# Kernel optimization log

Hardware: AMD Instinct MI355X
Metric: run time of the kernel (lower is better)

The kernel has to match this reference:

```python
import jax, jax.numpy as jnp
import numpy as np


def conv1x1(x, w, b):
    # 1x1 Conv2d: x [B,C,H,W], w [O,C], b [O] -> [B,O,H,W]
    return jnp.einsum('bchw,oc->bohw', x, w) + b[None, :, None, None]


def setup_inputs() -> dict:
    key = jax.random.key(0)
    ks = jax.random.split(key, 10)
    B, C, Ci, H, W = 4, 64, 32, 64, 64
    s = 0.05
    return {
        'supp_feature': jax.random.normal(ks[0], (B, C, H, W), jnp.float32),
        'ref_feature': jax.random.normal(ks[1], (B, C, H, W), jnp.float32),
        'theta_w': jax.random.normal(ks[2], (Ci, C), jnp.float32) * s,
        'theta_b': jax.random.normal(ks[3], (Ci,), jnp.float32) * s,
        'phi_w': jax.random.normal(ks[4], (Ci, C), jnp.float32) * s,
        'phi_b': jax.random.normal(ks[5], (Ci,), jnp.float32) * s,
        'g_w': jax.random.normal(ks[6], (Ci, C), jnp.float32) * s,
        'g_b': jax.random.normal(ks[7], (Ci,), jnp.float32) * s,
        'w_w': jax.random.normal(ks[8], (C, Ci), jnp.float32) * s,
        'w_b': jax.random.normal(ks[9], (C,), jnp.float32) * s,
    }


def reference(supp_feature, ref_feature, theta_w, theta_b, phi_w, phi_b,
              g_w, g_b, w_w, w_b):
    B, C, H, W = supp_feature.shape
    Ci = theta_w.shape[0]
    N = H * W
    theta_x = conv1x1(supp_feature, theta_w, theta_b).reshape(B, Ci, N)  # [B,Ci,N]
    phi_y = conv1x1(ref_feature, phi_w, phi_b).reshape(B, Ci, N)        # [B,Ci,M]
    g_y = conv1x1(ref_feature, g_w, g_b).reshape(B, Ci, N)              # [B,Ci,M]
    # f[b,n,m] = <theta_x[b,:,n], phi_y[b,:,m]>  (unscaled)
    f = jnp.einsum('bcn,bcm->bnm', theta_x, phi_y)
    # NOTE: softmax over dim=1 (the QUERY axis n), matching F.softmax(f, dim=1)
    f_div_C = jax.nn.softmax(f, axis=1)
    # x1[b,c,n] = sum_m f_div_C[b,n,m] * g_y[b,c,m]
    x1 = jnp.einsum('bnm,bcm->bcn', f_div_C, g_y).reshape(B, Ci, H, W)
    z = supp_feature + conv1x1(x1, w_w, w_b)
    return z
```

## Files before the change

kernel.cpp:

```cpp
#include <hip/hip_runtime.h>

#define C_ 64
#define CI_ 32
#define N_ 4096
#define LOG2E 1.4426950408889634f
#define NBLK 256

typedef __attribute__((ext_vector_type(8))) short bf16x8;
typedef __attribute__((ext_vector_type(4))) float f32x4;

__device__ __forceinline__ unsigned short f2bf_rne(float f) {
  unsigned u = __builtin_bit_cast(unsigned, f);
  unsigned r = (u + 0x7FFFu + ((u >> 16) & 1u)) >> 16;
  return (unsigned short)r;
}
__device__ __forceinline__ unsigned pack_bf2(float lo, float hi) {
  unsigned a = (__builtin_bit_cast(unsigned, lo) + 0x8000u) >> 16;
  unsigned b = (__builtin_bit_cast(unsigned, hi) + 0x8000u) & 0xFFFF0000u;
  return a | b;
}
__device__ __forceinline__ void dma16(const void* gp, const void* lp) {
  __builtin_amdgcn_global_load_lds(
      (const __attribute__((address_space(1))) unsigned*)(unsigned long long)gp,
      (__attribute__((address_space(3))) unsigned*)(unsigned)(unsigned long long)lp,
      16, 0, 0);
}

__device__ __forceinline__ void sync_grid(unsigned* base) {
  asm volatile("s_waitcnt vmcnt(0)" ::: "memory");
  __syncthreads();
  if (threadIdx.x == 0) {
    const int g = blockIdx.x & 7;
    __threadfence();
    __hip_atomic_fetch_add(&base[g * 32], 1u, __ATOMIC_RELAXED, __HIP_MEMORY_SCOPE_AGENT);
    unsigned sp = 0;
    if (blockIdx.x < 8) {
      while (__hip_atomic_load(&base[g * 32], __ATOMIC_RELAXED, __HIP_MEMORY_SCOPE_AGENT) < 32u) {
        __builtin_amdgcn_s_sleep(16);
        if (++sp > 60000u) break;
      }
      __hip_atomic_fetch_add(&base[512], 1u, __ATOMIC_RELAXED, __HIP_MEMORY_SCOPE_AGENT);
      sp = 0;
      while (__hip_atomic_load(&base[512], __ATOMIC_RELAXED, __HIP_MEMORY_SCOPE_AGENT) < 8u) {
        __builtin_amdgcn_s_sleep(16);
        if (++sp > 60000u) break;
      }
      __hip_atomic_store(&base[256 + g * 32], 1u, __ATOMIC_RELAXED, __HIP_MEMORY_SCOPE_AGENT);
    } else {
      while (__hip_atomic_load(&base[256 + g * 32], __ATOMIC_RELAXED, __HIP_MEMORY_SCOPE_AGENT) == 0u) {
        __builtin_amdgcn_s_sleep(16);
        if (++sp > 60000u) break;
      }
    }
  }
  __syncthreads();
}

__global__ __launch_bounds__(1024) void fused(
    const float* __restrict__ supp, const float* __restrict__ ref,
    const float* __restrict__ tw, const float* __restrict__ tb,
    const float* __restrict__ pw, const float* __restrict__ pb,
    const float* __restrict__ gw, const float* __restrict__ gb,
    const float* __restrict__ ww, const float* __restrict__ wb,
    unsigned short* __restrict__ theta, unsigned short* __restrict__ phi2,
    unsigned short* __restrict__ g2, float* __restrict__ den,
    unsigned short* __restrict__ ww2, unsigned* __restrict__ bar,
    float* __restrict__ out)
{
  __shared__ __align__(16) unsigned char LB[86016];
  const int tid = threadIdx.x;
  const int bid = blockIdx.x;
  const int lane = tid & 63;
  const int w = tid >> 6;
  const int row16 = lane & 15;
  const int quad = lane >> 4;

  {
    const int b = bid >> 6;
    const int n0 = (bid & 63) << 6;
    const int n = n0 + lane;
    float (*gL)[66] = (float (*)[66])LB;

    if (w < 12) {
      const int o = __builtin_amdgcn_readfirstlane(w & 3);
      const float *W, *bias, *src;
      if (w < 4)      { W = tw; bias = tb; src = supp; }
      else if (w < 8) { W = pw; bias = pb; src = ref; }
      else            { W = gw; bias = gb; src = ref; }
      const float* x = src + (size_t)b * (C_ * N_) + n;
      const float* Wo = W + o * 8 * C_;
      float acc[8];
#pragma unroll
      for (int k = 0; k < 8; k++) acc[k] = bias[o * 8 + k];
#pragma unroll 8
      for (int c = 0; c < C_; c++) {
        float v = x[(size_t)c * N_];
#pragma unroll
        for (int k = 0; k < 8; k++) acc[k] = fmaf(Wo[k * C_ + c], v, acc[k]);
      }
      if (w < 4) {
        unsigned pk[4];
#pragma unroll
        for (int k = 0; k < 4; k++)
          pk[k] = (unsigned)f2bf_rne(acc[2 * k] * LOG2E) |
                  ((unsigned)f2bf_rne(acc[2 * k + 1] * LOG2E) << 16);
        *(uint4*)(theta + (((size_t)b * N_ + n) << 5) + o * 8) = *(uint4*)pk;
      } else if (w < 8) {
        unsigned pk[4];
#pragma unroll
        for (int k = 0; k < 4; k++)
          pk[k] = (unsigned)f2bf_rne(acc[2 * k]) |
                  ((unsigned)f2bf_rne(acc[2 * k + 1]) << 16);
        size_t off = (((size_t)b * 128 + (n >> 5)) << 10) + o * 256 + (n & 31) * 8;
        *(uint4*)(phi2 + off) = *(uint4*)pk;
      } else {
#pragma unroll
        for (int k = 0; k < 8; k++) gL[o * 8 + k][lane] = acc[k];
      }
    } else if (bid == 16) {
      for (int e = tid - 768; e < C_ * CI_; e += 256) {
        int p = e & 31;
        int i = 4 * ((p >> 3) & 3) + (p & 3) + 16 * ((p >> 2) & 1);
        ww2[e] = f2bf_rne(ww[(e >> 5) * CI_ + i]);
      }
    }
    __syncthreads();
    if (tid < 256) {
      const int c = tid >> 7;
      const int rr2 = tid & 127;
      const int q = rr2 >> 5;
      const int i = rr2 & 31;
      const float* g0 = &gL[i][c * 32 + 4 * q];
      unsigned gk[4];
      gk[0] = pack_bf2(g0[0], g0[1]);
      gk[1] = pack_bf2(g0[2], g0[3]);
      gk[2] = pack_bf2(g0[16], g0[17]);
      gk[3] = pack_bf2(g0[18], g0[19]);
      size_t goff = (((size_t)b * 128 + (n0 >> 5) + c) << 10) + rr2 * 8;
      *(uint4*)(g2 + goff) = *(uint4*)gk;
    }
  }

  sync_grid(bar);

  {
    const int b = bid >> 6;
    const int mt = bid & 63;
    const int nq = w >> 2;
    const int ws = w & 3;
    unsigned short (*TH)[2][4096] = (unsigned short (*)[2][4096])LB;
    float* denL = (float*)(LB + 65536);

    bf16x8 bf = *(const bf16x8*)(phi2 +
        (((size_t)b * 128 + mt * 2 + (ws >> 1)) << 10) + (quad << 8) +
        ((ws & 1) * 16 + row16) * 8);

    const unsigned short* thbase = theta + (((size_t)b * N_ + nq * 1024) << 5);

#pragma unroll
    for (int s = 0; s < 2; s++)
      dma16(thbase + (ws * 2 + s) * 512 + lane * 8, &TH[nq][0][(ws * 2 + s) * 512]);
    __syncthreads();

    f32x4 zero = {0.f, 0.f, 0.f, 0.f};
    float ds4[4] = {0.f, 0.f, 0.f, 0.f};

    for (int ph = 0; ph < 8; ph++) {
      const int buf = ph & 1;
      if (ph + 1 < 8) {
#pragma unroll
        for (int s = 0; s < 2; s++)
          dma16(thbase + (ph + 1) * 4096 + (ws * 2 + s) * 512 + lane * 8,
                &TH[nq][buf ^ 1][(ws * 2 + s) * 512]);
      }
#pragma unroll
      for (int s = 0; s < 8; s++) {
        bf16x8 af = *(const bf16x8*)(&TH[nq][buf][s * 512 + row16 * 32 + quad * 8]);
        f32x4 ff = __builtin_amdgcn_mfma_f32_16x16x32_bf16(af, bf, zero, 0, 0, 0);
#pragma unroll
        for (int r = 0; r < 4; r++) ds4[r] += __builtin_amdgcn_exp2f(ff[r]);
      }
      __syncthreads();
    }

    float v = (ds4[0] + ds4[1]) + (ds4[2] + ds4[3]);
    v += __shfl_xor(v, 16);
    v += __shfl_xor(v, 32);
    if (lane < 16) denL[nq * 64 + ws * 16 + lane] = v;
    __syncthreads();
    if (tid < 64) {
      float sv = (denL[tid] + denL[64 + tid]) + (denL[128 + tid] + denL[192 + tid]);
      int ch = mt * 2 + (tid >> 5);
      int local = tid & 31;
      int qq = (local & 15) >> 2;
      int j = (local & 3) | (((local >> 4) & 1) << 2);
      den[(((size_t)b * 128 + ch) << 5) + 8 * qq + j] = sv;
    }
  }

  sync_grid(bar + 640);

  {
    const int p = bid;
    const int b = (p & 7) >> 1;
    const int t = ((p >> 3) << 1) | (p & 1);
    const int n0 = t << 6;
    const int ns = w & 3;
    const int q = w >> 2;
    unsigned short (*SB)[4][4096] = (unsigned short (*)[4][4096])LB;
    float* ldL = (float*)(LB + 65536);

    for (int e = tid; e < 4096; e += 1024)
      ldL[e] = -__log2f(den[((size_t)b << 12) + e]);

    bf16x8 tB = *(const bf16x8*)(theta +
        (((size_t)b * N_ + n0 + ns * 16 + row16) << 5) + (quad << 3));

    const size_t chb = (size_t)b * 128;
    const int sq = q;

    f32x4 zero = {0.f, 0.f, 0.f, 0.f};
    f32x4 xa = zero, xb = zero;

#pragma unroll
    for (int s = 0; s < 2; s++) {
      int idx = w * 2 + s;
      int cc = (idx >> 2) & 1;
      int part = idx & 3;
      const unsigned short* src = (part >= 2 ? g2 : phi2) +
          ((chb + sq * 32 + cc) << 10) + ((size_t)(part & 1) << 9) + lane * 8;
      dma16(src, &SB[0][sq][cc * 2048 + (part >= 2 ? 1024 : 0) + ((part & 1) << 9)]);
    }
    __syncthreads();

    for (int ph = 0; ph < 16; ph++) {
      const int buf = ph & 1;
      if (ph + 1 < 16) {
#pragma unroll
        for (int s = 0; s < 2; s++) {
          int idx = w * 2 + s;
          int cc = (idx >> 2) & 1;
          int part = idx & 3;
          const unsigned short* src = (part >= 2 ? g2 : phi2) +
              ((chb + sq * 32 + (ph + 1) * 2 + cc) << 10) + ((size_t)(part & 1) << 9) + lane * 8;
          dma16(src, &SB[buf ^ 1][sq][cc * 2048 + (part >= 2 ? 1024 : 0) + ((part & 1) << 9)]);
        }
      }
#pragma unroll
      for (int cc = 0; cc < 2; cc++) {
        const unsigned short* base = &SB[buf][q][cc * 2048];
        bf16x8 pA0 = *(const bf16x8*)(base + (quad << 8) + row16 * 8);
        bf16x8 pA1 = *(const bf16x8*)(base + (quad << 8) + (row16 + 16) * 8);
        bf16x8 gA0 = *(const bf16x8*)(base + 1024 + (quad << 8) + row16 * 8);
        bf16x8 gA1 = *(const bf16x8*)(base + 1024 + (quad << 8) + (row16 + 16) * 8);
        const float* lp = &ldL[((q * 32 + ph * 2 + cc) << 5) + (quad << 3)];
        f32x4 l0 = *(const f32x4*)lp;
        f32x4 l1 = *(const f32x4*)(lp + 4);

        f32x4 f0 = __builtin_amdgcn_mfma_f32_16x16x32_bf16(pA0, tB, l0, 0, 0, 0);
        f32x4 f1 = __builtin_amdgcn_mfma_f32_16x16x32_bf16(pA1, tB, l1, 0, 0, 0);

        uint4 d;
        d.x = pack_bf2(__builtin_amdgcn_exp2f(f0[0]), __builtin_amdgcn_exp2f(f0[1]));
        d.y = pack_bf2(__builtin_amdgcn_exp2f(f0[2]), __builtin_amdgcn_exp2f(f0[3]));
        d.z = pack_bf2(__builtin_amdgcn_exp2f(f1[0]), __builtin_amdgcn_exp2f(f1[1]));
        d.w = pack_bf2(__builtin_amdgcn_exp2f(f1[2]), __builtin_amdgcn_exp2f(f1[3]));
        bf16x8 Pb = __builtin_bit_cast(bf16x8, d);

        xa = __builtin_amdgcn_mfma_f32_16x16x32_bf16(gA0, Pb, xa, 0, 0, 0);
        xb = __builtin_amdgcn_mfma_f32_16x16x32_bf16(gA1, Pb, xb, 0, 0, 0);
      }
      __syncthreads();
    }

    float* part = (float*)LB;
    if (q) {
      float* dst = part + ((((q - 1) * 4 + ns) * 64 + lane) << 3);
#pragma unroll
      for (int r = 0; r < 4; r++) { dst[r] = xa[r]; dst[4 + r] = xb[r]; }
    }
    __syncthreads();
    if (q == 0) {
#pragma unroll
      for (int e = 0; e < 3; e++) {
        const float* s = part + (((e * 4 + ns) * 64 + lane) << 3);
#pragma unroll
        for (int r = 0; r < 4; r++) { xa[r] += s[r]; xb[r] += s[4 + r]; }
      }
      uint4 d;
      d.x = pack_bf2(xa[0], xa[1]);
      d.y = pack_bf2(xa[2], xa[3]);
      d.z = pack_bf2(xb[0], xb[1]);
      d.w = pack_bf2(xb[2], xb[3]);
      bf16x8 Bx = __builtin_bit_cast(bf16x8, d);
      const int nloc = n0 + ns * 16 + row16;
#pragma unroll
      for (int ct = 0; ct < 4; ct++) {
        bf16x8 aw = *(const bf16x8*)(ww2 + (ct * 16 + row16) * CI_ + (quad << 3));
        f32x4 o = __builtin_amdgcn_mfma_f32_16x16x32_bf16(aw, Bx, zero, 0, 0, 0);
#pragma unroll
        for (int r = 0; r < 4; r++) {
          int c = ct * 16 + quad * 4 + r;
          size_t ob = ((size_t)b * C_ + c) * N_ + nloc;
          out[ob] = o[r] + wb[c] + supp[ob];
        }
      }
    }
  }
}

extern "C" void kernel_launch(void* const* d_in, const int* in_sizes, int n_in,
                              void* d_out, int out_size, void* d_ws, size_t ws_size,
                              hipStream_t stream)
{
  const float* supp = (const float*)d_in[0];
  const float* ref  = (const float*)d_in[1];
  const float* tw   = (const float*)d_in[2];
  const float* tb   = (const float*)d_in[3];
  const float* pw   = (const float*)d_in[4];
  const float* pb   = (const float*)d_in[5];
  const float* gw   = (const float*)d_in[6];
  const float* gb   = (const float*)d_in[7];
  const float* ww   = (const float*)d_in[8];
  const float* wb   = (const float*)d_in[9];
  float* out = (float*)d_out;

  char* ws = (char*)d_ws;
  unsigned short* theta = (unsigned short*)ws;
  unsigned short* phi2  = (unsigned short*)(ws + (1u << 20));
  unsigned short* g2    = (unsigned short*)(ws + (2u << 20));
  float*          den   = (float*)(ws + (3u << 20));
  unsigned short* ww2   = (unsigned short*)(ws + (3u << 20) + 65536);
  unsigned*       bar   = (unsigned*)(ws + (3u << 20) + 65536 + 4096);

  hipMemsetAsync(bar, 0, 2 * 640 * sizeof(unsigned), stream);
  hipLaunchKernelGGL(fused, dim3(NBLK), dim3(1024), 0, stream,
                     supp, ref, tw, tb, pw, pb, gw, gb, ww, wb,
                     theta, phi2, g2, den, ww2, bar, out);
}
```

Baseline: 128.4 us.

## Add per-XCC fence stage to grid barrier and prefetch before second sync

Reworks the grid barrier. The per-block __threadfence is dropped, and one elected block per XCC waits for the release flag, issues a single fence and then joins a second counting round before blocks are released. Sleep intervals are shortened. The second barrier now comes after the first phi/g DMA and the theta load are issued, so those loads overlap the barrier wait. The extra barrier round adds latency and depends on the hardware XCC ID register, and issuing the theta load before the barrier may read data written by other blocks before it is visible.

```diff
diff --git a/kernel.cpp b/kernel.cpp
--- a/kernel.cpp
+++ b/kernel.cpp
@@ -26,30 +26,51 @@
       16, 0, 0);
 }
 
+#define A_ADD(p, v) __hip_atomic_fetch_add((p), (v), __ATOMIC_RELAXED, __HIP_MEMORY_SCOPE_AGENT)
+#define A_LD(p)     __hip_atomic_load((p), __ATOMIC_RELAXED, __HIP_MEMORY_SCOPE_AGENT)
+#define A_ST(p, v)  __hip_atomic_store((p), (v), __ATOMIC_RELAXED, __HIP_MEMORY_SCOPE_AGENT)
+
 __device__ __forceinline__ void sync_grid(unsigned* base) {
   asm volatile("s_waitcnt vmcnt(0)" ::: "memory");
   __syncthreads();
   if (threadIdx.x == 0) {
     const int g = blockIdx.x & 7;
-    __threadfence();
-    __hip_atomic_fetch_add(&base[g * 32], 1u, __ATOMIC_RELAXED, __HIP_MEMORY_SCOPE_AGENT);
+    A_ADD(&base[g * 32], 1u);
+    unsigned xcc;
+    asm volatile("s_getreg_b32 %0, hwreg(HW_REG_XCC_ID)" : "=s"(xcc));
+    unsigned exp0 = 0u;
+    const bool winner = __hip_atomic_compare_exchange_strong(
+        &base[544 + (xcc & 7) * 32], &exp0, 1u,
+        __ATOMIC_RELAXED, __ATOMIC_RELAXED, __HIP_MEMORY_SCOPE_AGENT);
     unsigned sp = 0;
     if (blockIdx.x < 8) {
-      while (__hip_atomic_load(&base[g * 32], __ATOMIC_RELAXED, __HIP_MEMORY_SCOPE_AGENT) < 32u) {
-        __builtin_amdgcn_s_sleep(16);
-        if (++sp > 60000u) break;
-      }
-      __hip_atomic_fetch_add(&base[512], 1u, __ATOMIC_RELAXED, __HIP_MEMORY_SCOPE_AGENT);
+      while (A_LD(&base[g * 32]) < 32u) {
+        __builtin_amdgcn_s_sleep(2); if (++sp > 500000u) break;
+      }
+      A_ADD(&base[512], 1u);
       sp = 0;
-      while (__hip_atomic_load(&base[512], __ATOMIC_RELAXED, __HIP_MEMORY_SCOPE_AGENT) < 8u) {
-        __builtin_amdgcn_s_sleep(16);
-        if (++sp > 60000u) break;
-      }
-      __hip_atomic_store(&base[256 + g * 32], 1u, __ATOMIC_RELAXED, __HIP_MEMORY_SCOPE_AGENT);
+      while (A_LD(&base[512]) < 8u) {
+        __builtin_amdgcn_s_sleep(2); if (++sp > 500000u) break;
+      }
+      A_ST(&base[256 + g * 32], 1u);
+    }
+    if (winner) {
+      sp = 0;
+      while (A_LD(&base[256 + g * 32]) == 0u) {
+        __builtin_amdgcn_s_sleep(2); if (++sp > 500000u) break;
+      }
+      __threadfence();
+      A_ADD(&base[800], 1u);
+    }
+    sp = 0;
+    if (blockIdx.x < 8) {
+      while (A_LD(&base[800]) < 8u) {
+        __builtin_amdgcn_s_sleep(2); if (++sp > 500000u) break;
+      }
+      A_ST(&base[832 + g * 32], 1u);
     } else {
-      while (__hip_atomic_load(&base[256 + g * 32], __ATOMIC_RELAXED, __HIP_MEMORY_SCOPE_AGENT) == 0u) {
-        __builtin_amdgcn_s_sleep(16);
-        if (++sp > 60000u) break;
+      while (A_LD(&base[832 + g * 32]) == 0u) {
+        __builtin_amdgcn_s_sleep(2); if (++sp > 500000u) break;
       }
     }
   }
@@ -198,8 +219,6 @@
     }
   }
 
-  sync_grid(bar + 640);
-
   {
     const int p = bid;
     const int b = (p & 7) >> 1;
@@ -209,18 +228,8 @@
     const int q = w >> 2;
     unsigned short (*SB)[4][4096] = (unsigned short (*)[4][4096])LB;
     float* ldL = (float*)(LB + 65536);
-
-    for (int e = tid; e < 4096; e += 1024)
-      ldL[e] = -__log2f(den[((size_t)b << 12) + e]);
-
-    bf16x8 tB = *(const bf16x8*)(theta +
-        (((size_t)b * N_ + n0 + ns * 16 + row16) << 5) + (quad << 3));
-
     const size_t chb = (size_t)b * 128;
     const int sq = q;
-
-    f32x4 zero = {0.f, 0.f, 0.f, 0.f};
-    f32x4 xa = zero, xb = zero;
 
 #pragma unroll
     for (int s = 0; s < 2; s++) {
@@ -231,7 +240,17 @@
           ((chb + sq * 32 + cc) << 10) + ((size_t)(part & 1) << 9) + lane * 8;
       dma16(src, &SB[0][sq][cc * 2048 + (part >= 2 ? 1024 : 0) + ((part & 1) << 9)]);
     }
-    __syncthreads();
+    bf16x8 tB = *(const bf16x8*)(theta +
+        (((size_t)b * N_ + n0 + ns * 16 + row16) << 5) + (quad << 3));
+
+    sync_grid(bar + 1088);
+
+    for (int e = tid; e < 4096; e += 1024)
+      ldL[e] = -__log2f(den[((size_t)b << 12) + e]);
+    __syncthreads();
+
+    f32x4 zero = {0.f, 0.f, 0.f, 0.f};
+    f32x4 xa = zero, xb = zero;
 
     for (int ph = 0; ph < 16; ph++) {
       const int buf = ph & 1;
@@ -333,7 +352,7 @@
   unsigned short* ww2   = (unsigned short*)(ws + (3u << 20) + 65536);
   unsigned*       bar   = (unsigned*)(ws + (3u << 20) + 65536 + 4096);
 
-  hipMemsetAsync(bar, 0, 2 * 640 * sizeof(unsigned), stream);
+  hipMemsetAsync(bar, 0, 2 * 1088 * sizeof(unsigned), stream);
   hipLaunchKernelGGL(fused, dim3(NBLK), dim3(1024), 0, stream,
                      supp, ref, tw, tb, pw, pb, gw, gb, ww, wb,
                      theta, phi2, g2, den, ww2, bar, out);
```

Result: faster. 123.2 us (-4.1%).
